# Performance work log

Hardware: AMD Instinct MI355X
Metric: run time of the kernel (lower is better)

## Reference

```python
import jax, jax.numpy as jnp
import numpy as np

DIM = 768
HEADS = 12
HEAD_DIM = DIM // HEADS
EPS = 1e-6
LN_EPS = 1e-5


def setup_inputs() -> dict:
    key = jax.random.key(0)
    k1, k2, k3, k4 = jax.random.split(key, 4)
    x = jax.random.normal(k1, (8, 4096, DIM), dtype=jnp.float32)
    ln_gamma = jnp.ones((DIM,), dtype=jnp.float32)
    ln_beta = jnp.zeros((DIM,), dtype=jnp.float32)
    # torch nn.Linear weight layout: [out_features, in_features]
    w_qkv = jax.random.normal(k2, (3 * DIM, DIM), dtype=jnp.float32) * (1.0 / np.sqrt(DIM))
    w_proj = jax.random.normal(k3, (DIM, DIM), dtype=jnp.float32) * (1.0 / np.sqrt(DIM))
    b_proj = jax.random.normal(k4, (DIM,), dtype=jnp.float32) * 0.01
    return {"x": x, "ln_gamma": ln_gamma, "ln_beta": ln_beta,
            "w_qkv": w_qkv, "w_proj": w_proj, "b_proj": b_proj}


def _elu1(t):
    return jax.nn.elu(t) + 1.0


def reference(x, ln_gamma, ln_beta, w_qkv, w_proj, b_proj):
    bsz, n, dim = x.shape
    # LayerNorm
    mu = jnp.mean(x, axis=-1, keepdims=True)
    var = jnp.mean(jnp.square(x - mu), axis=-1, keepdims=True)
    y = (x - mu) * jax.lax.rsqrt(var + LN_EPS) * ln_gamma + ln_beta
    # qkv projection: [b, n, 3*dim]
    qkv = jnp.einsum('bnd,ed->bne', y, w_qkv)
    qkv = qkv.reshape(bsz, n, 3, HEADS, HEAD_DIM)
    qkv = jnp.transpose(qkv, (2, 0, 3, 1, 4))  # [3, b, h, n, hd]
    q, k, v = _elu1(qkv[0]), _elu1(qkv[1]), qkv[2]
    # kv outer-product sum over tokens: [b, h, d, e]
    kv = jnp.einsum('bhnd,bhne->bhde', k, v)
    k_sum = jnp.sum(k, axis=2)                              # [b, h, d]
    z = 1.0 / (jnp.einsum('bhnd,bhd->bhn', q, k_sum) + EPS)  # [b, h, n]
    out = jnp.einsum('bhnd,bhde->bhne', q, kv) * z[..., None]
    out = jnp.transpose(out, (0, 2, 1, 3)).reshape(bsz, n, dim)
    return jnp.einsum('bnd,ed->bne', out, w_proj) + b_proj
```

## Files before the change

kernel.cpp:

```cpp
#include <hip/hip_runtime.h>
#include <stdint.h>

typedef __bf16 bf16;
typedef __bf16 bf16x4 __attribute__((ext_vector_type(4)));
typedef __bf16 bf16x8 __attribute__((ext_vector_type(8)));
typedef float  f32x4  __attribute__((ext_vector_type(4)));

#define DIM   768
#define HEADS 12
#define HD    64
#define SEQ   4096
#define NKT2  12

__device__ __forceinline__ void gload16(const void* g, void* l) {
  typedef const __attribute__((address_space(1))) uint32_t* gp_t;
  typedef __attribute__((address_space(3))) uint32_t* lp_t;
  gp_t gp = reinterpret_cast<gp_t>(reinterpret_cast<uintptr_t>(g));
  lp_t lp = reinterpret_cast<lp_t>(reinterpret_cast<uintptr_t>(l));
  __builtin_amdgcn_global_load_lds(gp, lp, 16, 0, 0);
}

__global__ __launch_bounds__(256) void wcvt_kernel(const float* __restrict__ src,
                                                   bf16* __restrict__ dst) {
  int i = (blockIdx.x * 256 + threadIdx.x) * 4;
  float4 v = *reinterpret_cast<const float4*>(src + i);
  bf16x4 o;
  o[0] = (bf16)v.x; o[1] = (bf16)v.y; o[2] = (bf16)v.z; o[3] = (bf16)v.w;
  *reinterpret_cast<bf16x4*>(dst + i) = o;
}

__global__ __launch_bounds__(256) void ln_kernel(const float* __restrict__ x,
    const float* __restrict__ gam, const float* __restrict__ bet,
    bf16* __restrict__ y) {
  const int tid = threadIdx.x, w = tid >> 6, l = tid & 63;
  const int row = blockIdx.x * 4 + w;
  const float* xr = x + (long)row * DIM;
  float4 v[3];
  float s = 0.f, ss = 0.f;
#pragma unroll
  for (int j = 0; j < 3; j++) {
    v[j] = *reinterpret_cast<const float4*>(xr + l * 4 + j * 256);
    s  += v[j].x + v[j].y + v[j].z + v[j].w;
    ss += v[j].x * v[j].x + v[j].y * v[j].y + v[j].z * v[j].z + v[j].w * v[j].w;
  }
#pragma unroll
  for (int m = 1; m < 64; m <<= 1) { s += __shfl_xor(s, m); ss += __shfl_xor(ss, m); }
  const float mu = s * (1.f / 768.f);
  const float rstd = rsqrtf(ss * (1.f / 768.f) - mu * mu + 1e-5f);
  bf16* yr = y + (long)row * DIM;
#pragma unroll
  for (int j = 0; j < 3; j++) {
    int c = l * 4 + j * 256;
    float4 g4 = *reinterpret_cast<const float4*>(gam + c);
    float4 b4 = *reinterpret_cast<const float4*>(bet + c);
    bf16x4 o;
    o[0] = (bf16)((v[j].x - mu) * rstd * g4.x + b4.x);
    o[1] = (bf16)((v[j].y - mu) * rstd * g4.y + b4.y);
    o[2] = (bf16)((v[j].z - mu) * rstd * g4.z + b4.z);
    o[3] = (bf16)((v[j].w - mu) * rstd * g4.w + b4.w);
    *reinterpret_cast<bf16x4*>(yr + c) = o;
  }
}

template <int MODE>
__global__ __launch_bounds__(512, 4) void gemm_kernel(
    const bf16* __restrict__ A, const bf16* __restrict__ Bw,
    bf16* __restrict__ qb, bf16* __restrict__ kb, bf16* __restrict__ vb,
    float* __restrict__ outp, const float* __restrict__ bias) {
  __shared__ __align__(16) char lds[32768];
  const int tid = threadIdx.x;
  const int wid = tid >> 6, l = tid & 63;
  const int wr = wid >> 2, wc = wid & 3;
  const int l16 = l & 15, l4 = l >> 4;

  const int NT = (MODE == 0) ? 18 : 6;
  const int nwg = NT * 256;
  const int orig = blockIdx.x;
  const int wgid = (orig & 7) * (nwg >> 3) + (orig >> 3);
  const int mt = wgid / NT, nt = wgid % NT;

  const int L0 = tid * 16, L1 = 8192 + tid * 16;
  const int r0 = L0 >> 7, s0 = (L0 >> 4) & 7;
  const int r1 = L1 >> 7, s1 = (L1 >> 4) & 7;
  const bf16* pA0 = A + (long)(mt * 128 + r0) * DIM + (s0 ^ (r0 & 7)) * 8;
  const bf16* pA1 = A + (long)(mt * 128 + r1) * DIM + (s1 ^ (r1 & 7)) * 8;
  const bf16* pB0 = Bw + (long)(nt * 128 + r0) * DIM + (s0 ^ (r0 & 7)) * 8;
  const bf16* pB1 = Bw + (long)(nt * 128 + r1) * DIM + (s1 ^ (r1 & 7)) * 8;

  int offA[2][4], offB[2][2];
#pragma unroll
  for (int ks = 0; ks < 2; ks++) {
#pragma unroll
    for (int mi = 0; mi < 4; mi++) {
      int row = wr * 64 + mi * 16 + l16;
      offA[ks][mi] = row * 128 + (((l4 + 4 * ks) ^ (l16 & 7)) << 4);
    }
#pragma unroll
    for (int ni = 0; ni < 2; ni++) {
      int row = wc * 32 + ni * 16 + l16;
      offB[ks][ni] = 16384 + row * 128 + (((l4 + 4 * ks) ^ (l16 & 7)) << 4);
    }
  }

  f32x4 acc[4][2];
#pragma unroll
  for (int m = 0; m < 4; m++)
#pragma unroll
    for (int n = 0; n < 2; n++) { f32x4 z4 = {0.f, 0.f, 0.f, 0.f}; acc[m][n] = z4; }

  for (int t = 0; t < NKT2; t++) {
    __syncthreads();
    gload16(pA0 + t * 64, lds + L0);
    gload16(pA1 + t * 64, lds + L1);
    gload16(pB0 + t * 64, lds + 16384 + L0);
    gload16(pB1 + t * 64, lds + 16384 + L1);
    __syncthreads();
#pragma unroll
    for (int ks = 0; ks < 2; ks++) {
      bf16x8 a[4], b[2];
#pragma unroll
      for (int mi = 0; mi < 4; mi++)
        a[mi] = *reinterpret_cast<const bf16x8*>(lds + offA[ks][mi]);
#pragma unroll
      for (int ni = 0; ni < 2; ni++)
        b[ni] = *reinterpret_cast<const bf16x8*>(lds + offB[ks][ni]);
#pragma unroll
      for (int mi = 0; mi < 4; mi++)
#pragma unroll
        for (int ni = 0; ni < 2; ni++)
          acc[mi][ni] = __builtin_amdgcn_mfma_f32_16x16x32_bf16(a[mi], b[ni], acc[mi][ni], 0, 0, 0);
    }
  }

  if constexpr (MODE == 0) {
    bf16* Cs = (bf16*)lds;
    const int s = nt / 6;
    const int j = nt % 6;
    bf16* dst0 = (s == 0) ? qb : (s == 1) ? kb : vb;
    __syncthreads();
#pragma unroll
    for (int mi = 0; mi < 4; mi++)
#pragma unroll
      for (int ni = 0; ni < 2; ni++)
#pragma unroll
        for (int i = 0; i < 4; i++) {
          float val = acc[mi][ni][i];
          if (s < 2) val = val > 0.f ? val + 1.f : __expf(val);
          Cs[(wr * 64 + mi * 16 + l4 * 4 + i) * 128 + wc * 32 + ni * 16 + l16] = (bf16)val;
        }
    __syncthreads();
#pragma unroll
    for (int it = 0; it < 4; it++) {
      int bi = it * 8192 + tid * 16;
      int row = bi >> 8;
      int col = (bi & 255) >> 1;
      int h = j * 2 + (col >> 6), d = col & 63;
      int trow = mt * 128 + row;
      int bb = trow >> 12, tok = trow & 4095;
      *reinterpret_cast<bf16x8*>(dst0 +
          ((long)(bb * HEADS + h) * SEQ + tok) * HD + d) =
          *reinterpret_cast<const bf16x8*>(Cs + (bi >> 1));
    }
  } else {
#pragma unroll
    for (int ni = 0; ni < 2; ni++) {
      int col = nt * 128 + wc * 32 + ni * 16 + l16;
      float bv = bias[col];
#pragma unroll
      for (int mi = 0; mi < 4; mi++)
#pragma unroll
        for (int i = 0; i < 4; i++) {
          long trow = mt * 128 + wr * 64 + mi * 16 + l4 * 4 + i;
          outp[trow * DIM + col] = acc[mi][ni][i] + bv;
        }
    }
  }
}

__global__ __launch_bounds__(256) void kv_kernel(
    const bf16* __restrict__ kb, const bf16* __restrict__ vb,
    float* __restrict__ kv_part, float* __restrict__ ks_part) {
  __shared__ __align__(16) union UU {
    struct { bf16 Ks[128 * 64]; bf16 Vs[128 * 64]; } s;
    float red[8192];
  } u;
  __shared__ float ksred[4][64];
  const int head = blockIdx.x, sp = blockIdx.y;
  const int tid = threadIdx.x, w = tid >> 6, l = tid & 63;
  const int d0 = (l >> 3) * 8, e0 = (l & 7) * 8;
  const bf16* K = kb + (long)(head * SEQ + sp * 512) * HD;
  const bf16* V = vb + (long)(head * SEQ + sp * 512) * HD;
  float acc[8][8];
#pragma unroll
  for (int i = 0; i < 8; i++)
#pragma unroll
    for (int jj = 0; jj < 8; jj++) acc[i][jj] = 0.f;
  float ks[8] = {0.f, 0.f, 0.f, 0.f, 0.f, 0.f, 0.f, 0.f};

  for (int t0 = 0; t0 < 512; t0 += 128) {
    __syncthreads();
#pragma unroll
    for (int r = 0; r < 4; r++) {
      gload16(K + t0 * 64 + r * 2048 + tid * 8, u.s.Ks + r * 2048 + tid * 8);
      gload16(V + t0 * 64 + r * 2048 + tid * 8, u.s.Vs + r * 2048 + tid * 8);
    }
    __syncthreads();
    for (int n = w * 32; n < w * 32 + 32; n++) {
      bf16x8 k8 = *reinterpret_cast<const bf16x8*>(u.s.Ks + n * 64 + d0);
      bf16x8 v8 = *reinterpret_cast<const bf16x8*>(u.s.Vs + n * 64 + e0);
      float kf[8], vf[8];
#pragma unroll
      for (int i = 0; i < 8; i++) { kf[i] = (float)k8[i]; vf[i] = (float)v8[i]; }
#pragma unroll
      for (int i = 0; i < 8; i++) {
        ks[i] += kf[i];
#pragma unroll
        for (int jj = 0; jj < 8; jj++) acc[i][jj] += kf[i] * vf[jj];
      }
    }
  }
  if ((l & 7) == 0) {
#pragma unroll
    for (int i = 0; i < 8; i++) ksred[w][d0 + i] = ks[i];
  }
  __syncthreads();
  if (w >= 2) {
    float* dst = u.red + (w - 2) * 4096;
#pragma unroll
    for (int i = 0; i < 8; i++) {
      f32x4 a = {acc[i][0], acc[i][1], acc[i][2], acc[i][3]};
      f32x4 b = {acc[i][4], acc[i][5], acc[i][6], acc[i][7]};
      *reinterpret_cast<f32x4*>(dst + (d0 + i) * 64 + e0) = a;
      *reinterpret_cast<f32x4*>(dst + (d0 + i) * 64 + e0 + 4) = b;
    }
  }
  __syncthreads();
  if (w < 2) {
    const float* src = u.red + w * 4096;
#pragma unroll
    for (int i = 0; i < 8; i++)
#pragma unroll
      for (int jj = 0; jj < 8; jj++) acc[i][jj] += src[(d0 + i) * 64 + e0 + jj];
  }
  __syncthreads();
  if (w == 1) {
    float* dst = u.red;
#pragma unroll
    for (int i = 0; i < 8; i++) {
      f32x4 a = {acc[i][0], acc[i][1], acc[i][2], acc[i][3]};
      f32x4 b = {acc[i][4], acc[i][5], acc[i][6], acc[i][7]};
      *reinterpret_cast<f32x4*>(dst + (d0 + i) * 64 + e0) = a;
      *reinterpret_cast<f32x4*>(dst + (d0 + i) * 64 + e0 + 4) = b;
    }
  }
  __syncthreads();
  if (w == 0) {
    const float* src = u.red;
#pragma unroll
    for (int i = 0; i < 8; i++)
#pragma unroll
      for (int jj = 0; jj < 8; jj++) acc[i][jj] += src[(d0 + i) * 64 + e0 + jj];
    float* dst = kv_part + (long)(head * 8 + sp) * 4096;
#pragma unroll
    for (int i = 0; i < 8; i++) {
      f32x4 a = {acc[i][0], acc[i][1], acc[i][2], acc[i][3]};
      f32x4 b = {acc[i][4], acc[i][5], acc[i][6], acc[i][7]};
      *reinterpret_cast<f32x4*>(dst + (d0 + i) * 64 + e0) = a;
      *reinterpret_cast<f32x4*>(dst + (d0 + i) * 64 + e0 + 4) = b;
    }
  }
  if (tid < 64)
    ks_part[(head * 8 + sp) * 64 + tid] =
        ksred[0][tid] + ksred[1][tid] + ksred[2][tid] + ksred[3][tid];
}

__global__ __launch_bounds__(256) void kvfin_kernel(const float* __restrict__ kv_part,
    const float* __restrict__ ks_part, bf16* __restrict__ kvT, float* __restrict__ ksum) {
  const int head = blockIdx.x, tid = threadIdx.x;
  const long base = (long)head * 8 * 4096;
  const int d = tid >> 2, ecol = (tid & 3) * 16;
  float s[16];
#pragma unroll
  for (int q = 0; q < 16; q++) s[q] = 0.f;
  for (int sp = 0; sp < 8; sp++) {
    const float* p = kv_part + base + sp * 4096 + d * 64 + ecol;
#pragma unroll
    for (int q = 0; q < 16; q++) s[q] += p[q];
  }
#pragma unroll
  for (int q = 0; q < 16; q++) kvT[head * 4096 + (ecol + q) * 64 + d] = (bf16)s[q];
  if (tid < 64) {
    float t = 0.f;
    for (int sp = 0; sp < 8; sp++) t += ks_part[(head * 8 + sp) * 64 + tid];
    ksum[head * 64 + tid] = t;
  }
}

__global__ __launch_bounds__(256) void qout_kernel(const bf16* __restrict__ qb,
    const bf16* __restrict__ kvT, const float* __restrict__ ksum,
    bf16* __restrict__ outp) {
  __shared__ __align__(16) bf16 Qs[128 * 64];
  __shared__ __align__(16) bf16 Bs2[64 * 64];
  __shared__ float ksum_s[64];
  __shared__ float z_s[128];
  const int head = blockIdx.x, tt = blockIdx.y;
  const int b = head / HEADS, h = head % HEADS;
  const int tid = threadIdx.x, w = tid >> 6, l = tid & 63;
  const int l16 = l & 15, l4 = l >> 4;
  const bf16* Qg = qb + (long)(head * SEQ + tt * 128) * HD;
#pragma unroll
  for (int r = 0; r < 4; r++) gload16(Qg + r * 2048 + tid * 8, Qs + r * 2048 + tid * 8);
#pragma unroll
  for (int r = 0; r < 2; r++)
    gload16(kvT + head * 4096 + r * 2048 + tid * 8, Bs2 + r * 2048 + tid * 8);
  if (tid < 64) ksum_s[tid] = ksum[head * 64 + tid];
  __syncthreads();
  if (tid < 128) {
    float dsum = 0.f;
#pragma unroll
    for (int i = 0; i < 8; i++) {
      bf16x8 q8 = *reinterpret_cast<const bf16x8*>(Qg + tid * 64 + i * 8);
#pragma unroll
      for (int jj = 0; jj < 8; jj++) dsum += (float)q8[jj] * ksum_s[i * 8 + jj];
    }
    z_s[tid] = 1.f / (dsum + 1e-6f);
  }
  f32x4 acc[2][4];
#pragma unroll
  for (int m = 0; m < 2; m++)
#pragma unroll
    for (int n = 0; n < 4; n++) { f32x4 z4 = {0.f, 0.f, 0.f, 0.f}; acc[m][n] = z4; }
#pragma unroll
  for (int kk = 0; kk < 2; kk++) {
    bf16x8 af[2], bfr[4];
#pragma unroll
    for (int m = 0; m < 2; m++)
      af[m] = *reinterpret_cast<const bf16x8*>(Qs + (w * 32 + m * 16 + l16) * 64 + kk * 32 + l4 * 8);
#pragma unroll
    for (int n = 0; n < 4; n++)
      bfr[n] = *reinterpret_cast<const bf16x8*>(Bs2 + (n * 16 + l16) * 64 + kk * 32 + l4 * 8);
#pragma unroll
    for (int m = 0; m < 2; m++)
#pragma unroll
      for (int n = 0; n < 4; n++)
        acc[m][n] = __builtin_amdgcn_mfma_f32_16x16x32_bf16(af[m], bfr[n], acc[m][n], 0, 0, 0);
  }
  __syncthreads();
#pragma unroll
  for (int m = 0; m < 2; m++)
#pragma unroll
    for (int n = 0; n < 4; n++)
#pragma unroll
      for (int i = 0; i < 4; i++) {
        int row = w * 32 + m * 16 + l4 * 4 + i;
        Qs[row * 64 + n * 16 + l16] = (bf16)(acc[m][n][i] * z_s[row]);
      }
  __syncthreads();
#pragma unroll
  for (int r = 0; r < 4; r++) {
    int idx = r * 2048 + tid * 8;
    int row = idx >> 6, col = idx & 63;
    *reinterpret_cast<bf16x8*>(outp + (long)(b * SEQ + tt * 128 + row) * DIM + h * HD + col) =
        *reinterpret_cast<const bf16x8*>(Qs + idx);
  }
}

extern "C" void kernel_launch(void* const* d_in, const int* in_sizes, int n_in,
                              void* d_out, int out_size, void* d_ws, size_t ws_size,
                              hipStream_t stream) {
  const float* x     = (const float*)d_in[0];
  const float* gam   = (const float*)d_in[1];
  const float* bet   = (const float*)d_in[2];
  const float* wqkv  = (const float*)d_in[3];
  const float* wproj = (const float*)d_in[4];
  const float* bproj = (const float*)d_in[5];
  float* out = (float*)d_out;
  char* ws = (char*)d_ws;

  bf16*  y       = (bf16*)(ws);
  bf16*  qb      = (bf16*)(ws + 50331648);
  bf16*  kb      = (bf16*)(ws + 100663296);
  bf16*  vb      = (bf16*)(ws + 150994944);
  bf16*  wqkv_b  = (bf16*)(ws + 201326592);
  bf16*  wproj_b = (bf16*)(ws + 204865536);
  float* kv_part = (float*)(ws + 206045184);
  float* ks_part = (float*)(ws + 218628096);
  bf16*  kvT     = (bf16*)(ws + 218824704);
  float* ksum    = (float*)(ws + 219611136);

  wcvt_kernel<<<1728, 256, 0, stream>>>(wqkv, wqkv_b);
  wcvt_kernel<<<576, 256, 0, stream>>>(wproj, wproj_b);
  ln_kernel<<<8192, 256, 0, stream>>>(x, gam, bet, y);
  gemm_kernel<0><<<dim3(18 * 256), 512, 0, stream>>>(y, wqkv_b, qb, kb, vb, nullptr, nullptr);
  kv_kernel<<<dim3(96, 8), 256, 0, stream>>>(kb, vb, kv_part, ks_part);
  kvfin_kernel<<<96, 256, 0, stream>>>(kv_part, ks_part, kvT, ksum);
  qout_kernel<<<dim3(96, 32), 256, 0, stream>>>(qb, kvT, ksum, y);
  gemm_kernel<1><<<dim3(6 * 256), 512, 0, stream>>>(y, wproj_b, nullptr, nullptr, nullptr, out, bproj);
}
```

Baseline: 293.0 us.

## Store K/V transposed and compute KV outer product with MFMA

The QKV GEMM epilogue now writes K and V in a transposed [head, dim, token] layout through a swizzled LDS staging buffer. This lets the kv kernel load token-contiguous tiles and compute the K^T V outer-product sum with bf16 MFMA instructions instead of scalar FMA loops, which also removes the multi-wave LDS reduction. The attention kernel computes its normaliser from the Q tile already in LDS using all threads plus a shuffle, rather than re-reading Q from global memory. The transposed epilogue does scalar LDS gathers and per-token-strided global writes, which may cost more than the old row-wise stores.

```diff
diff --git a/kernel.cpp b/kernel.cpp
--- a/kernel.cpp
+++ b/kernel.cpp
@@ -133,33 +133,66 @@
   }
 
   if constexpr (MODE == 0) {
-    bf16* Cs = (bf16*)lds;
     const int s = nt / 6;
     const int j = nt % 6;
-    bf16* dst0 = (s == 0) ? qb : (s == 1) ? kb : vb;
-    __syncthreads();
-#pragma unroll
-    for (int mi = 0; mi < 4; mi++)
-#pragma unroll
-      for (int ni = 0; ni < 2; ni++)
-#pragma unroll
-        for (int i = 0; i < 4; i++) {
-          float val = acc[mi][ni][i];
-          if (s < 2) val = val > 0.f ? val + 1.f : __expf(val);
-          Cs[(wr * 64 + mi * 16 + l4 * 4 + i) * 128 + wc * 32 + ni * 16 + l16] = (bf16)val;
+    if (s == 0) {
+      bf16* Cs = (bf16*)lds;
+      __syncthreads();
+#pragma unroll
+      for (int mi = 0; mi < 4; mi++)
+#pragma unroll
+        for (int ni = 0; ni < 2; ni++)
+#pragma unroll
+          for (int i = 0; i < 4; i++) {
+            float val = acc[mi][ni][i];
+            val = val > 0.f ? val + 1.f : __expf(val);
+            Cs[(wr * 64 + mi * 16 + l4 * 4 + i) * 128 + wc * 32 + ni * 16 + l16] = (bf16)val;
+          }
+      __syncthreads();
+#pragma unroll
+      for (int it = 0; it < 4; it++) {
+        int bi = it * 8192 + tid * 16;
+        int row = bi >> 8;
+        int col = (bi & 255) >> 1;
+        int h = j * 2 + (col >> 6), d = col & 63;
+        int trow = mt * 128 + row;
+        int bb = trow >> 12, tok = trow & 4095;
+        *reinterpret_cast<bf16x8*>(qb +
+            ((long)(bb * HEADS + h) * SEQ + tok) * HD + d) =
+            *reinterpret_cast<const bf16x8*>(Cs + (bi >> 1));
+      }
+    } else {
+      bf16* dst0 = (s == 1) ? kb : vb;
+      __syncthreads();
+#pragma unroll
+      for (int mi = 0; mi < 4; mi++)
+#pragma unroll
+        for (int ni = 0; ni < 2; ni++)
+#pragma unroll
+          for (int i = 0; i < 4; i++) {
+            float val = acc[mi][ni][i];
+            if (s == 1) val = val > 0.f ? val + 1.f : __expf(val);
+            int tr = wr * 64 + mi * 16 + l4 * 4 + i;
+            int cc = wc * 32 + ni * 16 + l16;
+            *reinterpret_cast<bf16*>(lds + tr * 256 + ((cc * 2) ^ ((tr & 7) << 4))) = (bf16)val;
+          }
+      __syncthreads();
+      const int cc = tid & 127;
+      const int sp2 = tid >> 7;
+      const int hh = j * 2 + (cc >> 6), dd = cc & 63;
+      const int bb = (mt * 128) >> 12;
+      const int n0 = ((mt * 128) & 4095) + sp2 * 32;
+      bf16* dstp = dst0 + ((long)(bb * HEADS + hh) * HD + dd) * SEQ + n0;
+#pragma unroll
+      for (int q8i = 0; q8i < 4; q8i++) {
+        bf16x8 o;
+#pragma unroll
+        for (int jj = 0; jj < 8; jj++) {
+          int tok = sp2 * 32 + q8i * 8 + jj;
+          o[jj] = *reinterpret_cast<const bf16*>(lds + tok * 256 + ((cc * 2) ^ ((tok & 7) << 4)));
         }
-    __syncthreads();
-#pragma unroll
-    for (int it = 0; it < 4; it++) {
-      int bi = it * 8192 + tid * 16;
-      int row = bi >> 8;
-      int col = (bi & 255) >> 1;
-      int h = j * 2 + (col >> 6), d = col & 63;
-      int trow = mt * 128 + row;
-      int bb = trow >> 12, tok = trow & 4095;
-      *reinterpret_cast<bf16x8*>(dst0 +
-          ((long)(bb * HEADS + h) * SEQ + tok) * HD + d) =
-          *reinterpret_cast<const bf16x8*>(Cs + (bi >> 1));
+        *reinterpret_cast<bf16x8*>(dstp + q8i * 8) = o;
+      }
     }
   } else {
 #pragma unroll
@@ -178,100 +211,101 @@
 }
 
 __global__ __launch_bounds__(256) void kv_kernel(
-    const bf16* __restrict__ kb, const bf16* __restrict__ vb,
+    const bf16* __restrict__ ktb, const bf16* __restrict__ vtb,
     float* __restrict__ kv_part, float* __restrict__ ks_part) {
-  __shared__ __align__(16) union UU {
-    struct { bf16 Ks[128 * 64]; bf16 Vs[128 * 64]; } s;
-    float red[8192];
-  } u;
-  __shared__ float ksred[4][64];
+  __shared__ __align__(16) char lds[32768];
   const int head = blockIdx.x, sp = blockIdx.y;
-  const int tid = threadIdx.x, w = tid >> 6, l = tid & 63;
-  const int d0 = (l >> 3) * 8, e0 = (l & 7) * 8;
-  const bf16* K = kb + (long)(head * SEQ + sp * 512) * HD;
-  const bf16* V = vb + (long)(head * SEQ + sp * 512) * HD;
-  float acc[8][8];
-#pragma unroll
-  for (int i = 0; i < 8; i++)
-#pragma unroll
-    for (int jj = 0; jj < 8; jj++) acc[i][jj] = 0.f;
-  float ks[8] = {0.f, 0.f, 0.f, 0.f, 0.f, 0.f, 0.f, 0.f};
-
-  for (int t0 = 0; t0 < 512; t0 += 128) {
+  const int tid = threadIdx.x;
+  const int wid = tid >> 6, l = tid & 63;
+  const int wd = wid >> 1, we = wid & 1;
+  const int l16 = l & 15, l4 = l >> 4;
+
+  int offK[4][2], offV[4][2];
+#pragma unroll
+  for (int ks = 0; ks < 4; ks++) {
+#pragma unroll
+    for (int mi = 0; mi < 2; mi++) {
+      int row = wd * 32 + mi * 16 + l16;
+      offK[ks][mi] = row * 256 + ((ks * 64 + l4 * 16) ^ ((row & 7) << 4));
+    }
+#pragma unroll
+    for (int ni = 0; ni < 2; ni++) {
+      int row = we * 32 + ni * 16 + l16;
+      offV[ks][ni] = 16384 + row * 256 + ((ks * 64 + l4 * 16) ^ ((row & 7) << 4));
+    }
+  }
+  const bf16* srcK[4]; const bf16* srcV[4]; int ldst[4];
+#pragma unroll
+  for (int g = 0; g < 4; g++) {
+    int L = g * 4096 + tid * 16;
+    int r = L >> 8, cb = L & 255;
+    int ce = (cb ^ ((r & 7) << 4)) >> 1;
+    srcK[g] = ktb + ((long)head * HD + r) * SEQ + sp * 512 + ce;
+    srcV[g] = vtb + ((long)head * HD + r) * SEQ + sp * 512 + ce;
+    ldst[g] = L;
+  }
+
+  f32x4 acc[2][2];
+#pragma unroll
+  for (int m = 0; m < 2; m++)
+#pragma unroll
+    for (int n = 0; n < 2; n++) { f32x4 z4 = {0.f, 0.f, 0.f, 0.f}; acc[m][n] = z4; }
+  float ksf = 0.f;
+  const int ksd = tid >> 2, ksq = tid & 3;
+
+  for (int c = 0; c < 4; c++) {
     __syncthreads();
 #pragma unroll
-    for (int r = 0; r < 4; r++) {
-      gload16(K + t0 * 64 + r * 2048 + tid * 8, u.s.Ks + r * 2048 + tid * 8);
-      gload16(V + t0 * 64 + r * 2048 + tid * 8, u.s.Vs + r * 2048 + tid * 8);
+    for (int g = 0; g < 4; g++) {
+      gload16(srcK[g] + c * 128, lds + ldst[g]);
+      gload16(srcV[g] + c * 128, lds + 16384 + ldst[g]);
     }
     __syncthreads();
-    for (int n = w * 32; n < w * 32 + 32; n++) {
-      bf16x8 k8 = *reinterpret_cast<const bf16x8*>(u.s.Ks + n * 64 + d0);
-      bf16x8 v8 = *reinterpret_cast<const bf16x8*>(u.s.Vs + n * 64 + e0);
-      float kf[8], vf[8];
-#pragma unroll
-      for (int i = 0; i < 8; i++) { kf[i] = (float)k8[i]; vf[i] = (float)v8[i]; }
-#pragma unroll
-      for (int i = 0; i < 8; i++) {
-        ks[i] += kf[i];
-#pragma unroll
-        for (int jj = 0; jj < 8; jj++) acc[i][jj] += kf[i] * vf[jj];
+#pragma unroll
+    for (int q = 0; q < 4; q++) {
+      bf16x8 k8 = *reinterpret_cast<const bf16x8*>(
+          lds + ksd * 256 + ((ksq * 64 + q * 16) ^ ((ksd & 7) << 4)));
+#pragma unroll
+      for (int jj = 0; jj < 8; jj++) ksf += (float)k8[jj];
+    }
+#pragma unroll
+    for (int ks = 0; ks < 4; ks++) {
+      bf16x8 a[2], b[2];
+      a[0] = *reinterpret_cast<const bf16x8*>(lds + offK[ks][0]);
+      a[1] = *reinterpret_cast<const bf16x8*>(lds + offK[ks][1]);
+      b[0] = *reinterpret_cast<const bf16x8*>(lds + offV[ks][0]);
+      b[1] = *reinterpret_cast<const bf16x8*>(lds + offV[ks][1]);
+#pragma unroll
+      for (int mi = 0; mi < 2; mi++)
+#pragma unroll
+        for (int ni = 0; ni < 2; ni++)
+          acc[mi][ni] = __builtin_amdgcn_mfma_f32_16x16x32_bf16(a[mi], b[ni], acc[mi][ni], 0, 0, 0);
+    }
+  }
+  ksf += __shfl_xor(ksf, 1);
+  ksf += __shfl_xor(ksf, 2);
+  if (ksq == 0) ks_part[(head * 8 + sp) * 64 + ksd] = ksf;
+
+  __syncthreads();
+#pragma unroll
+  for (int mi = 0; mi < 2; mi++)
+#pragma unroll
+    for (int ni = 0; ni < 2; ni++)
+#pragma unroll
+      for (int i = 0; i < 4; i++) {
+        int dd = wd * 32 + mi * 16 + l4 * 4 + i;
+        int ee = we * 32 + ni * 16 + l16;
+        *reinterpret_cast<float*>(lds + dd * 256 + ((ee * 4) ^ ((dd & 7) << 4))) = acc[mi][ni][i];
       }
-    }
-  }
-  if ((l & 7) == 0) {
-#pragma unroll
-    for (int i = 0; i < 8; i++) ksred[w][d0 + i] = ks[i];
-  }
   __syncthreads();
-  if (w >= 2) {
-    float* dst = u.red + (w - 2) * 4096;
-#pragma unroll
-    for (int i = 0; i < 8; i++) {
-      f32x4 a = {acc[i][0], acc[i][1], acc[i][2], acc[i][3]};
-      f32x4 b = {acc[i][4], acc[i][5], acc[i][6], acc[i][7]};
-      *reinterpret_cast<f32x4*>(dst + (d0 + i) * 64 + e0) = a;
-      *reinterpret_cast<f32x4*>(dst + (d0 + i) * 64 + e0 + 4) = b;
-    }
-  }
-  __syncthreads();
-  if (w < 2) {
-    const float* src = u.red + w * 4096;
-#pragma unroll
-    for (int i = 0; i < 8; i++)
-#pragma unroll
-      for (int jj = 0; jj < 8; jj++) acc[i][jj] += src[(d0 + i) * 64 + e0 + jj];
-  }
-  __syncthreads();
-  if (w == 1) {
-    float* dst = u.red;
-#pragma unroll
-    for (int i = 0; i < 8; i++) {
-      f32x4 a = {acc[i][0], acc[i][1], acc[i][2], acc[i][3]};
-      f32x4 b = {acc[i][4], acc[i][5], acc[i][6], acc[i][7]};
-      *reinterpret_cast<f32x4*>(dst + (d0 + i) * 64 + e0) = a;
-      *reinterpret_cast<f32x4*>(dst + (d0 + i) * 64 + e0 + 4) = b;
-    }
-  }
-  __syncthreads();
-  if (w == 0) {
-    const float* src = u.red;
-#pragma unroll
-    for (int i = 0; i < 8; i++)
-#pragma unroll
-      for (int jj = 0; jj < 8; jj++) acc[i][jj] += src[(d0 + i) * 64 + e0 + jj];
-    float* dst = kv_part + (long)(head * 8 + sp) * 4096;
-#pragma unroll
-    for (int i = 0; i < 8; i++) {
-      f32x4 a = {acc[i][0], acc[i][1], acc[i][2], acc[i][3]};
-      f32x4 b = {acc[i][4], acc[i][5], acc[i][6], acc[i][7]};
-      *reinterpret_cast<f32x4*>(dst + (d0 + i) * 64 + e0) = a;
-      *reinterpret_cast<f32x4*>(dst + (d0 + i) * 64 + e0 + 4) = b;
-    }
-  }
-  if (tid < 64)
-    ks_part[(head * 8 + sp) * 64 + tid] =
-        ksred[0][tid] + ksred[1][tid] + ksred[2][tid] + ksred[3][tid];
+  float* dst = kv_part + (long)(head * 8 + sp) * 4096;
+  const int dd2 = tid >> 2, eq = tid & 3;
+#pragma unroll
+  for (int q = 0; q < 4; q++) {
+    f32x4 v4 = *reinterpret_cast<const f32x4*>(
+        lds + dd2 * 256 + ((eq * 64 + q * 16) ^ ((dd2 & 7) << 4)));
+    *reinterpret_cast<f32x4*>(dst + dd2 * 64 + eq * 16 + q * 4) = v4;
+  }
 }
 
 __global__ __launch_bounds__(256) void kvfin_kernel(const float* __restrict__ kv_part,
@@ -315,15 +349,17 @@
     gload16(kvT + head * 4096 + r * 2048 + tid * 8, Bs2 + r * 2048 + tid * 8);
   if (tid < 64) ksum_s[tid] = ksum[head * 64 + tid];
   __syncthreads();
-  if (tid < 128) {
+  {
+    const int tok = tid >> 1, hf = tid & 1;
     float dsum = 0.f;
 #pragma unroll
-    for (int i = 0; i < 8; i++) {
-      bf16x8 q8 = *reinterpret_cast<const bf16x8*>(Qg + tid * 64 + i * 8);
-#pragma unroll
-      for (int jj = 0; jj < 8; jj++) dsum += (float)q8[jj] * ksum_s[i * 8 + jj];
-    }
-    z_s[tid] = 1.f / (dsum + 1e-6f);
+    for (int q = 0; q < 4; q++) {
+      bf16x8 q8 = *reinterpret_cast<const bf16x8*>(Qs + tok * 64 + hf * 32 + q * 8);
+#pragma unroll
+      for (int jj = 0; jj < 8; jj++) dsum += (float)q8[jj] * ksum_s[hf * 32 + q * 8 + jj];
+    }
+    dsum += __shfl_xor(dsum, 1);
+    if (hf == 0) z_s[tok] = 1.f / (dsum + 1e-6f);
   }
   f32x4 acc[2][4];
 #pragma unroll
```

Measured after the change: 269.8 us. 1.09x faster.
